# Optimization experiments

Measured on AMD Instinct MI355X. Metric: run time of the kernel, lower is better.

The kernel has to match this reference:

```python
import jax, jax.numpy as jnp
import numpy as np


def setup_inputs() -> dict:
    key = jax.random.key(0)
    ks = jax.random.split(key, 7)
    B, S, D_IN, D_K, D_V = 4, 4096, 1024, 64, 64
    s = 1.0 / np.sqrt(D_IN)
    return {
        "query": jax.random.normal(ks[0], (B, S, D_IN), jnp.float32),
        "key": jax.random.normal(ks[1], (B, S, D_IN), jnp.float32),
        "value": jax.random.normal(ks[2], (B, S, D_IN), jnp.float32),
        "Wq": jax.random.normal(ks[3], (D_IN, D_K), jnp.float32) * s,
        "bq": jnp.zeros((D_K,), jnp.float32),
        "Wk": jax.random.normal(ks[4], (D_IN, D_K), jnp.float32) * s,
        "bk": jnp.zeros((D_K,), jnp.float32),
        "Wv": jax.random.normal(ks[5], (D_IN, D_V), jnp.float32) * s,
        "bv": jnp.zeros((D_V,), jnp.float32),
    }


def reference(query, key, value, Wq, bq, Wk, bk, Wv, bv):
    # q(query) is computed twice in the original but is identical; compute once.
    q = query @ Wq + bq            # [B,S,dk]
    k = key @ Wk + bk              # [B,S,dk]
    v = value @ Wv + bv            # [B,S,dv]
    scale = jnp.asarray(q.shape[-1] ** 0.5, q.dtype)
    scores = jnp.einsum("bqd,bkd->bqk", q, k) / scale  # [B,S,S]
    probs = jax.nn.softmax(scores, axis=-1)
    return jnp.einsum("bqk,bkd->bqd", probs, v)        # [B,S,dv]
```

## Files before the change

kernel.cpp:

```cpp
#include <hip/hip_runtime.h>
#include <cmath>

constexpr int B_  = 4;
constexpr int S_  = 4096;
constexpr int DIN = 1024;
constexpr int DH  = 64;

typedef short bf16x8 __attribute__((ext_vector_type(8)));
typedef float f32x4  __attribute__((ext_vector_type(4)));

#define GPTR(p) (const __attribute__((address_space(1))) unsigned int*)(p)
#define LPTR(p) (__attribute__((address_space(3))) unsigned int*)(p)

__device__ __forceinline__ ushort f2bf(float x) {
    unsigned int u = __float_as_uint(x);
    return (ushort)((u + 0x7FFFu + ((u >> 16) & 1u)) >> 16);
}

__device__ __forceinline__ bf16x8 cvt8(float4 a, float4 b) {
    union { bf16x8 v; ushort u[8]; } r;
    r.u[0] = f2bf(a.x); r.u[1] = f2bf(a.y); r.u[2] = f2bf(a.z); r.u[3] = f2bf(a.w);
    r.u[4] = f2bf(b.x); r.u[5] = f2bf(b.y); r.u[6] = f2bf(b.z); r.u[7] = f2bf(b.w);
    return r.v;
}

#define QSCALE 0.18033688011112042f

__global__ __launch_bounds__(256) void setup_w(
    const float* __restrict__ Wq, const float* __restrict__ Wk,
    const float* __restrict__ Wv, ushort* __restrict__ Wt_g)
{
    const int y = blockIdx.y;
    const float* W = (y == 0) ? Wq : (y == 1) ? Wk : Wv;
    const int g   = blockIdx.x * 256 + threadIdx.x;
    const int p   = g & 7;
    const int n   = (g >> 3) & 63;
    const int win = g >> 9;
    const int c   = p ^ (n & 7);
    const int k0  = win * 64 + c * 8;
    union { uint4 q; ushort u[8]; } r;
    #pragma unroll
    for (int i = 0; i < 8; ++i) r.u[i] = f2bf(W[(size_t)(k0 + i) * DH + n]);
    *(uint4*)(Wt_g + ((size_t)y << 16) + (size_t)(((win * 64 + n) * 8 + p) * 8)) = r.q;
}

__global__ __launch_bounds__(256) void proj_kernel(
    const float* __restrict__ Xq, const float* __restrict__ Xk, const float* __restrict__ Xv,
    const float* __restrict__ bq, const float* __restrict__ bk, const float* __restrict__ bv,
    const ushort* __restrict__ Wt_g,
    ushort* __restrict__ Qb, ushort* __restrict__ Kb, ushort* __restrict__ Vt)
{
    const int y = blockIdx.y;
    const float *X, *bias;
    if (y == 0)      { X = Xq; bias = bq; }
    else if (y == 1) { X = Xk; bias = bk; }
    else             { X = Xv; bias = bv; }

    __shared__ ushort Wlds[2][4096];

    const int tid  = threadIdx.x;
    const int w    = tid >> 6;
    const int lane = tid & 63;
    const int m    = lane & 15;
    const int quad = lane >> 4;
    const int row0 = blockIdx.x * 64;

    const size_t  xrow = (size_t)(row0 + w * 16 + m) * DIN;
    const ushort* wsrc = Wt_g + ((size_t)y << 16);

    float bias_v[4];
    #pragma unroll
    for (int nt = 0; nt < 4; ++nt) bias_v[nt] = bias[nt * 16 + m];

    f32x4 acc[4] = {};

    #pragma unroll
    for (int i = 0; i < 2; ++i) {
        const int chunk = w * 2 + i;
        __builtin_amdgcn_global_load_lds(GPTR(wsrc + chunk * 512 + lane * 8),
                                         LPTR(&Wlds[0][chunk * 512]), 16, 0, 0);
    }
    float4 cur[4], nxt[4];
    {
        const float* px = X + xrow + quad * 8;
        cur[0] = *(const float4*)(px);      cur[1] = *(const float4*)(px + 4);
        cur[2] = *(const float4*)(px + 32); cur[3] = *(const float4*)(px + 36);
    }
    __syncthreads();

    for (int it = 0; it < 16; ++it) {
        if (it < 15) {
            #pragma unroll
            for (int i = 0; i < 2; ++i) {
                const int chunk = w * 2 + i;
                __builtin_amdgcn_global_load_lds(
                    GPTR(wsrc + (it + 1) * 4096 + chunk * 512 + lane * 8),
                    LPTR(&Wlds[(it + 1) & 1][chunk * 512]), 16, 0, 0);
            }
            const float* px = X + xrow + (it + 1) * 64 + quad * 8;
            nxt[0] = *(const float4*)(px);      nxt[1] = *(const float4*)(px + 4);
            nxt[2] = *(const float4*)(px + 32); nxt[3] = *(const float4*)(px + 36);
        }
        const ushort* buf = Wlds[it & 1];
        #pragma unroll
        for (int ks = 0; ks < 2; ++ks) {
            const bf16x8 a = cvt8(cur[ks * 2], cur[ks * 2 + 1]);
            #pragma unroll
            for (int nt = 0; nt < 4; ++nt) {
                const int n = nt * 16 + m;
                const int p = (ks * 4 + quad) ^ (m & 7);
                const bf16x8 bfr = *(const bf16x8*)&buf[n * 64 + p * 8];
                acc[nt] = __builtin_amdgcn_mfma_f32_16x16x32_bf16(a, bfr, acc[nt], 0, 0, 0);
            }
        }
        __syncthreads();
        #pragma unroll
        for (int i = 0; i < 4; ++i) cur[i] = nxt[i];
    }

    if (y < 2) {
        ushort* Out = (y == 0) ? Qb : Kb;
        const float sc = (y == 0) ? QSCALE : 1.0f;
        #pragma unroll
        for (int nt = 0; nt < 4; ++nt)
            #pragma unroll
            for (int j = 0; j < 4; ++j) {
                const int row = row0 + w * 16 + quad * 4 + j;
                Out[(size_t)row * DH + nt * 16 + m] = f2bf((acc[nt][j] + bias_v[nt]) * sc);
            }
    } else {
        ushort* Vx = (ushort*)Wlds;
        #pragma unroll
        for (int nt = 0; nt < 4; ++nt)
            #pragma unroll
            for (int j = 0; j < 4; ++j) {
                const int d = nt * 16 + m;
                const int s = w * 16 + quad * 4 + j;
                Vx[d * 72 + (((s >> 3) ^ (d & 7)) * 8) + (s & 7)] = f2bf(acc[nt][j] + bias_v[nt]);
            }
        __syncthreads();
        const int batch = row0 >> 12;
        const int s0    = row0 & 4095;
        for (int i = tid; i < 512; i += 256) {
            const int d = i >> 3, c = i & 7;
            const uint4 v = *(const uint4*)&Vx[d * 72 + ((c ^ (d & 7)) * 8)];
            *(uint4*)(Vt + ((size_t)batch * 64 + d) * S_ + s0 + c * 8) = v;
        }
    }
}

__global__ __launch_bounds__(256, 4) void attn_kernel(
    const ushort* __restrict__ Qb, const ushort* __restrict__ Kb,
    const ushort* __restrict__ Vt, float* __restrict__ Opart, float* __restrict__ Lpart)
{
    __shared__ ushort Ks[64 * 64];
    __shared__ ushort Vs[64 * 64];
    __shared__ ushort Pt[64 * 72];

    const int tid  = threadIdx.x;
    const int w    = tid >> 6;
    const int lane = tid & 63;
    const int m    = lane & 15;
    const int quad = lane >> 4;
    const int b    = blockIdx.z, jc = blockIdx.y, qt = blockIdx.x;
    const int q0   = qt * 64;

    bf16x8 qf[2];
    #pragma unroll
    for (int ks = 0; ks < 2; ++ks)
        qf[ks] = *(const bf16x8*)(Qb + (size_t)(b * S_ + q0 + w * 16 + m) * 64
                                     + ks * 32 + quad * 8);

    f32x4 acc_o[4] = {};
    float Lp[4] = {};

    const ushort* kbase = Kb + (size_t)b * S_ * 64;
    const ushort* vbase = Vt + (size_t)b * 64 * S_;

    for (int it = 0; it < 16; ++it) {
        const int jt = jc * 16 + it;
        __syncthreads();
        #pragma unroll
        for (int i = 0; i < 2; ++i) {
            const int slot = w * 128 + i * 64 + lane;
            const int j = slot >> 3, c = slot & 7;
            __builtin_amdgcn_global_load_lds(
                GPTR(kbase + (size_t)(jt * 64 + j) * 64 + ((c ^ (j & 7)) * 8)),
                LPTR(&Ks[(w * 128 + i * 64) * 8]), 16, 0, 0);
            __builtin_amdgcn_global_load_lds(
                GPTR(vbase + (size_t)j * S_ + jt * 64 + ((c ^ (j & 7)) * 8)),
                LPTR(&Vs[(w * 128 + i * 64) * 8]), 16, 0, 0);
        }
        __syncthreads();

        f32x4 acc_s[4] = {};
        #pragma unroll
        for (int ks = 0; ks < 2; ++ks)
            #pragma unroll
            for (int jt4 = 0; jt4 < 4; ++jt4) {
                const int j = jt4 * 16 + m;
                const bf16x8 kf = *(const bf16x8*)&Ks[j * 64 + (((ks * 4 + quad) ^ (j & 7)) * 8)];
                acc_s[jt4] = __builtin_amdgcn_mfma_f32_16x16x32_bf16(
                    qf[ks], kf, acc_s[jt4], 0, 0, 0);
            }

        #pragma unroll
        for (int jt4 = 0; jt4 < 4; ++jt4)
            #pragma unroll
            for (int r = 0; r < 4; ++r) {
                const float e = exp2f(acc_s[jt4][r]);
                Lp[r] += e;
                Pt[(w * 16 + quad * 4 + r) * 72 + jt4 * 16 + m] = f2bf(e);
            }

        #pragma unroll
        for (int jc2 = 0; jc2 < 2; ++jc2) {
            const bf16x8 pf = *(const bf16x8*)&Pt[(w * 16 + m) * 72 + jc2 * 32 + quad * 8];
            #pragma unroll
            for (int dt = 0; dt < 4; ++dt) {
                const int d = dt * 16 + m;
                const bf16x8 vf = *(const bf16x8*)&Vs[d * 64 + (((jc2 * 4 + quad) ^ (d & 7)) * 8)];
                acc_o[dt] = __builtin_amdgcn_mfma_f32_16x16x32_bf16(pf, vf, acc_o[dt], 0, 0, 0);
            }
        }
    }

    #pragma unroll
    for (int r = 0; r < 4; ++r) {
        float s = Lp[r];
        #pragma unroll
        for (int off = 1; off < 16; off <<= 1)
            s += __shfl_xor(s, off, 64);
        Lp[r] = s;
    }

    const size_t bj = (size_t)(b * 4 + jc);
    float* Ob = Opart + (bj << 18);
    #pragma unroll
    for (int dt = 0; dt < 4; ++dt)
        #pragma unroll
        for (int r = 0; r < 4; ++r) {
            const int row = q0 + w * 16 + quad * 4 + r;
            Ob[(size_t)row * 64 + dt * 16 + m] = acc_o[dt][r];
        }
    if (m == 0) {
        #pragma unroll
        for (int r = 0; r < 4; ++r)
            Lpart[bj * 4096 + q0 + w * 16 + quad * 4 + r] = Lp[r];
    }
}

__global__ __launch_bounds__(256) void reduce_kernel(
    const float* __restrict__ Opart, const float* __restrict__ Lpart, float* __restrict__ out)
{
    const int g    = blockIdx.x * 256 + threadIdx.x;
    const int base = g << 2;
    const int b    = base >> 18;
    const int rem  = base & 0x3FFFF;
    const int q    = rem >> 6;
    float4 o = make_float4(0.f, 0.f, 0.f, 0.f);
    float  l = 0.f;
    #pragma unroll
    for (int jcc = 0; jcc < 4; ++jcc) {
        const float4 p = *(const float4*)(Opart + (((size_t)(b * 4 + jcc)) << 18) + rem);
        o.x += p.x; o.y += p.y; o.z += p.z; o.w += p.w;
        l += Lpart[(size_t)(b * 4 + jcc) * 4096 + q];
    }
    const float inv = 1.0f / l;
    o.x *= inv; o.y *= inv; o.z *= inv; o.w *= inv;
    *(float4*)(out + base) = o;
}

extern "C" void kernel_launch(void* const* d_in, const int* in_sizes, int n_in,
                              void* d_out, int out_size, void* d_ws, size_t ws_size,
                              hipStream_t stream)
{
    const float* query = (const float*)d_in[0];
    const float* key_  = (const float*)d_in[1];
    const float* value = (const float*)d_in[2];
    const float* Wq    = (const float*)d_in[3];
    const float* bq    = (const float*)d_in[4];
    const float* Wk    = (const float*)d_in[5];
    const float* bk    = (const float*)d_in[6];
    const float* Wv    = (const float*)d_in[7];
    const float* bv    = (const float*)d_in[8];
    float* out = (float*)d_out;

    char* ws = (char*)d_ws;
    ushort* Qb    = (ushort*)(ws);
    ushort* Kb    = (ushort*)(ws + (2  << 20));
    ushort* Vt    = (ushort*)(ws + (4  << 20));
    float*  Opart = (float*) (ws + (6  << 20));
    float*  Lpart = (float*) (ws + (22 << 20));
    ushort* Wt_g  = (ushort*)(ws + (6  << 20));

    setup_w<<<dim3(32, 3), 256, 0, stream>>>(Wq, Wk, Wv, Wt_g);
    proj_kernel<<<dim3(256, 3), 256, 0, stream>>>(
        query, key_, value, bq, bk, bv, Wt_g, Qb, Kb, Vt);
    attn_kernel<<<dim3(64, 4, 4), 256, 0, stream>>>(Qb, Kb, Vt, Opart, Lpart);
    reduce_kernel<<<dim3(1024), 256, 0, stream>>>(Opart, Lpart, out);
}
```

Measured before the change: 261.4 us.

## Load projection weights directly into registers in MFMA fragment order

Weights are pre-packed so each lane's bf16x8 B-fragment sits contiguously in fragment order. The projection kernel then loads them straight from global memory into registers with double buffering, instead of staging them through LDS with per-iteration barriers. It also adds an occupancy hint of 3 blocks per CU. The cost is more register use and redundant global (L2) weight reads per wave, since every wave now fetches the whole weight tile itself.

New measurement: 271.0 us. 3.7% more time.

```diff
diff --git a/kernel.cpp b/kernel.cpp
--- a/kernel.cpp
+++ b/kernel.cpp
@@ -32,19 +32,22 @@
 {
     const int y = blockIdx.y;
     const float* W = (y == 0) ? Wq : (y == 1) ? Wk : Wv;
-    const int g   = blockIdx.x * 256 + threadIdx.x;
-    const int p   = g & 7;
-    const int n   = (g >> 3) & 63;
-    const int win = g >> 9;
-    const int c   = p ^ (n & 7);
-    const int k0  = win * 64 + c * 8;
+    const int g    = blockIdx.x * 256 + threadIdx.x;
+    const int lane = g & 63;
+    const int nt   = (g >> 6) & 3;
+    const int ks   = (g >> 8) & 1;
+    const int it   = g >> 9;
+    const int m    = lane & 15;
+    const int quad = lane >> 4;
+    const int n    = nt * 16 + m;
+    const int k0   = it * 64 + (ks * 4 + quad) * 8;
     union { uint4 q; ushort u[8]; } r;
     #pragma unroll
     for (int i = 0; i < 8; ++i) r.u[i] = f2bf(W[(size_t)(k0 + i) * DH + n]);
-    *(uint4*)(Wt_g + ((size_t)y << 16) + (size_t)(((win * 64 + n) * 8 + p) * 8)) = r.q;
-}
-
-__global__ __launch_bounds__(256) void proj_kernel(
+    *(uint4*)(Wt_g + ((size_t)y << 16) + (size_t)g * 8) = r.q;
+}
+
+__global__ __launch_bounds__(256, 3) void proj_kernel(
     const float* __restrict__ Xq, const float* __restrict__ Xk, const float* __restrict__ Xv,
     const float* __restrict__ bq, const float* __restrict__ bk, const float* __restrict__ bv,
     const ushort* __restrict__ Wt_g,
@@ -56,7 +59,7 @@
     else if (y == 1) { X = Xk; bias = bk; }
     else             { X = Xv; bias = bv; }
 
-    __shared__ ushort Wlds[2][4096];
+    __shared__ ushort Vx[64 * 72];
 
     const int tid  = threadIdx.x;
     const int w    = tid >> 6;
@@ -66,56 +69,44 @@
     const int row0 = blockIdx.x * 64;
 
     const size_t  xrow = (size_t)(row0 + w * 16 + m) * DIN;
-    const ushort* wsrc = Wt_g + ((size_t)y << 16);
+    const ushort* wsrc = Wt_g + ((size_t)y << 16) + (size_t)lane * 8;
 
     float bias_v[4];
     #pragma unroll
     for (int nt = 0; nt < 4; ++nt) bias_v[nt] = bias[nt * 16 + m];
 
     f32x4 acc[4] = {};
-
-    #pragma unroll
-    for (int i = 0; i < 2; ++i) {
-        const int chunk = w * 2 + i;
-        __builtin_amdgcn_global_load_lds(GPTR(wsrc + chunk * 512 + lane * 8),
-                                         LPTR(&Wlds[0][chunk * 512]), 16, 0, 0);
-    }
-    float4 cur[4], nxt[4];
+    float4 xb[2][4];
+    uint4  wb[2][8];
+
     {
         const float* px = X + xrow + quad * 8;
-        cur[0] = *(const float4*)(px);      cur[1] = *(const float4*)(px + 4);
-        cur[2] = *(const float4*)(px + 32); cur[3] = *(const float4*)(px + 36);
-    }
-    __syncthreads();
-
+        xb[0][0] = *(const float4*)(px);      xb[0][1] = *(const float4*)(px + 4);
+        xb[0][2] = *(const float4*)(px + 32); xb[0][3] = *(const float4*)(px + 36);
+        #pragma unroll
+        for (int f = 0; f < 8; ++f)
+            wb[0][f] = *(const uint4*)(wsrc + (size_t)f * 512);
+    }
+
+    #pragma unroll
     for (int it = 0; it < 16; ++it) {
+        const int cb = it & 1, nb = cb ^ 1;
         if (it < 15) {
-            #pragma unroll
-            for (int i = 0; i < 2; ++i) {
-                const int chunk = w * 2 + i;
-                __builtin_amdgcn_global_load_lds(
-                    GPTR(wsrc + (it + 1) * 4096 + chunk * 512 + lane * 8),
-                    LPTR(&Wlds[(it + 1) & 1][chunk * 512]), 16, 0, 0);
-            }
             const float* px = X + xrow + (it + 1) * 64 + quad * 8;
-            nxt[0] = *(const float4*)(px);      nxt[1] = *(const float4*)(px + 4);
-            nxt[2] = *(const float4*)(px + 32); nxt[3] = *(const float4*)(px + 36);
-        }
-        const ushort* buf = Wlds[it & 1];
+            xb[nb][0] = *(const float4*)(px);      xb[nb][1] = *(const float4*)(px + 4);
+            xb[nb][2] = *(const float4*)(px + 32); xb[nb][3] = *(const float4*)(px + 36);
+            #pragma unroll
+            for (int f = 0; f < 8; ++f)
+                wb[nb][f] = *(const uint4*)(wsrc + (size_t)((it + 1) * 8 + f) * 512);
+        }
         #pragma unroll
         for (int ks = 0; ks < 2; ++ks) {
-            const bf16x8 a = cvt8(cur[ks * 2], cur[ks * 2 + 1]);
-            #pragma unroll
-            for (int nt = 0; nt < 4; ++nt) {
-                const int n = nt * 16 + m;
-                const int p = (ks * 4 + quad) ^ (m & 7);
-                const bf16x8 bfr = *(const bf16x8*)&buf[n * 64 + p * 8];
-                acc[nt] = __builtin_amdgcn_mfma_f32_16x16x32_bf16(a, bfr, acc[nt], 0, 0, 0);
-            }
-        }
-        __syncthreads();
-        #pragma unroll
-        for (int i = 0; i < 4; ++i) cur[i] = nxt[i];
+            const bf16x8 a = cvt8(xb[cb][ks * 2], xb[cb][ks * 2 + 1]);
+            #pragma unroll
+            for (int nt = 0; nt < 4; ++nt)
+                acc[nt] = __builtin_amdgcn_mfma_f32_16x16x32_bf16(
+                    a, *(const bf16x8*)&wb[cb][ks * 4 + nt], acc[nt], 0, 0, 0);
+        }
     }
 
     if (y < 2) {
@@ -129,7 +120,6 @@
                 Out[(size_t)row * DH + nt * 16 + m] = f2bf((acc[nt][j] + bias_v[nt]) * sc);
             }
     } else {
-        ushort* Vx = (ushort*)Wlds;
         #pragma unroll
         for (int nt = 0; nt < 4; ++nt)
             #pragma unroll
```
